# Performance work log

Hardware: AMD Instinct MI355X
Metric: run time of the kernel (lower is better)

Reference implementation:

```python
import jax, jax.numpy as jnp
import numpy as np

B, N, U = 16, 512, 128          # batch, n_node, units
E = (3 + 1) * 2                 # n_edge = (n_gaze+1)*2 with n_gaze=3
N_STEP = 3


def setup_inputs() -> dict:
    key = jax.random.key(0)
    ks = jax.random.split(key, 6)
    init_state = jax.random.normal(ks[0], (B, N, U), dtype=jnp.float32)
    adj_matrix = jax.random.uniform(ks[1], (B, E, N, N), dtype=jnp.float32)
    # learned parameters (per build()): alpha ones, w ~ N(0, 0.02), b zeros
    alpha = jnp.ones((E,), dtype=jnp.float32)
    w = jax.random.normal(ks[2], (E, U, U), dtype=jnp.float32) * 0.02
    b = jnp.zeros((E, U), dtype=jnp.float32)
    # Keras GRUCell (reset_after=False): kernel [in, 3U], recurrent [U, 3U], bias [3U]
    gru_kernel = jax.random.normal(ks[3], (E * U, 3 * U), dtype=jnp.float32) * 0.02
    gru_rec_kernel = jax.random.normal(ks[4], (U, 3 * U), dtype=jnp.float32) * 0.02
    gru_bias = jnp.zeros((3 * U,), dtype=jnp.float32)
    return {"init_state": init_state, "adj_matrix": adj_matrix, "alpha": alpha,
            "w": w, "b": b, "gru_kernel": gru_kernel,
            "gru_rec_kernel": gru_rec_kernel, "gru_bias": gru_bias}


def _gru_cell(x, h, kernel, rec, bias):
    # Keras GRUCell, reset_after=False:
    # z = sigmoid(x Wz + h Uz); r = sigmoid(x Wr + h Ur)
    # hh = tanh(x Wh + (r*h) Uh); h' = z*h + (1-z)*hh
    m = x @ kernel + bias                      # [BN, 3U]
    xz, xr, xh = jnp.split(m, 3, axis=-1)
    z = jax.nn.sigmoid(xz + h @ rec[:, :U])
    r = jax.nn.sigmoid(xr + h @ rec[:, U:2 * U])
    hh = jnp.tanh(xh + (r * h) @ rec[:, 2 * U:])
    return z * h + (1.0 - z) * hh


def reference(init_state, adj_matrix, alpha, w, b, gru_kernel, gru_rec_kernel, gru_bias):
    # contribution-coefficient weighted adjacency: [B, E, N, N]
    wadj = adj_matrix * jax.nn.sigmoid(alpha)[None, :, None, None]
    state = init_state                         # [B, N, U]
    for _ in range(N_STEP):
        # per-edge transform: h[b,n,e,u] = state[b,n,:] @ w[e] + b[e]
        h = jnp.einsum('bnd,edu->bneu', state, w) + b          # [B, N, E, U]
        # adjacency aggregation for all edges at once (fused batched GEMM)
        neigh = jnp.einsum('benm,bmeu->bneu', wadj, h)         # [B, N, E, U]
        gru_in = neigh.reshape(B * N, E * U)
        gru_h = state.reshape(B * N, U)
        state = _gru_cell(gru_in, gru_h, gru_kernel, gru_rec_kernel, gru_bias).reshape(B, N, U)
    return state
```

## Files before the change

kernel.cpp:

```cpp
#include <hip/hip_runtime.h>


typedef __attribute__((ext_vector_type(8))) short short8;
typedef __attribute__((ext_vector_type(4))) short short4v;
typedef __attribute__((ext_vector_type(4))) float f32x4;

__device__ __forceinline__ short bfs(float f) {
    __bf16 h = (__bf16)f;
    return __builtin_bit_cast(short, h);
}
__device__ __forceinline__ void split2(float x, short& hi, short& lo) {
    __bf16 h = (__bf16)x;
    hi = __builtin_bit_cast(short, h);
    __bf16 l = (__bf16)(x - (float)h);
    lo = __builtin_bit_cast(short, l);
}
__device__ __forceinline__ float sigm(float x) { return 1.0f / (1.0f + __expf(-x)); }

#define LDP 40

#define MFMA3(acc, ah, al, bh, bl)                                             \
    acc = __builtin_amdgcn_mfma_f32_16x16x32_bf16(ah, bh, acc, 0, 0, 0);       \
    acc = __builtin_amdgcn_mfma_f32_16x16x32_bf16(al, bh, acc, 0, 0, 0);       \
    acc = __builtin_amdgcn_mfma_f32_16x16x32_bf16(ah, bl, acc, 0, 0, 0);

__global__ __launch_bounds__(256) void k_prep(const float* __restrict__ w,
                                              const float* __restrict__ gk,
                                              const float* __restrict__ grk,
                                              const float* __restrict__ alpha,
                                              const float* __restrict__ init_state,
                                              short* __restrict__ Wt_hi, short* __restrict__ Wt_lo,
                                              short* __restrict__ GKt_hi, short* __restrict__ GKt_lo,
                                              short* __restrict__ REC_hi, short* __restrict__ REC_lo,
                                              short* __restrict__ NG2_hi, short* __restrict__ NG2_lo,
                                              float* __restrict__ siga) {
    int idx = blockIdx.x * 256 + threadIdx.x;
    if (idx < 131072) {
        int e = idx >> 14, rem = idx & 16383, u = rem >> 7, d = rem & 127;
        split2(w[e * 16384 + d * 128 + u], Wt_hi[idx], Wt_lo[idx]);
    } else if (idx < 573440) {
        int i2 = idx - 131072;
        int c = i2 / 1152, k = i2 - c * 1152;
        float v = (k < 1024) ? gk[k * 384 + c]
                             : ((c < 256) ? grk[(k - 1024) * 384 + c] : 0.0f);
        split2(v, GKt_hi[i2], GKt_lo[i2]);
    } else if (idx < 589824) {
        int i2 = idx - 573440;
        int u = i2 >> 7, d = i2 & 127;
        split2(grk[d * 384 + 256 + u], REC_hi[i2], REC_lo[i2]);
    } else if (idx < 1638400) {
        int i2 = idx - 589824;
        int r = i2 >> 7, d = i2 & 127;
        split2(init_state[i2], NG2_hi[(size_t)r * 1152 + 1024 + d],
                              NG2_lo[(size_t)r * 1152 + 1024 + d]);
    } else if (idx < 1638408) {
        int e = idx - 1638400;
        siga[e] = sigm(alpha[e]);
    }
}

__global__ __launch_bounds__(256) void k_edge(const short* __restrict__ Wt_hi,
                                              const short* __restrict__ Wt_lo,
                                              const short* __restrict__ NG2_hi,
                                              const short* __restrict__ NG2_lo,
                                              const float* __restrict__ bias,
                                              const float* __restrict__ siga,
                                              short* __restrict__ Ht_hi,
                                              short* __restrict__ Ht_lo) {
    const int e = blockIdx.y;
    const int col0 = blockIdx.x * 128;
    __shared__ short Ash[128 * LDP], Asl[128 * LDP];
    __shared__ short Bsh[128 * LDP], Bsl[128 * LDP];
    const int tid = threadIdx.x;
    const int lane = tid & 63, wave = tid >> 6;
    const int wr = wave >> 1, wc = wave & 1;
    const int l15 = lane & 15, g8 = (lane >> 4) * 8;
    const short* wh = Wt_hi + e * 16384;
    const short* wl = Wt_lo + e * 16384;
    f32x4 acc[4][4] = {};
    for (int k0 = 0; k0 < 128; k0 += 32) {
        __syncthreads();
#pragma unroll
        for (int it = 0; it < 2; ++it) {
            int idx = tid + it * 256;
            int r = idx >> 2, gg = idx & 3;
            *(short8*)&Ash[r * LDP + gg * 8] = *(const short8*)&wh[r * 128 + k0 + gg * 8];
            *(short8*)&Asl[r * LDP + gg * 8] = *(const short8*)&wl[r * 128 + k0 + gg * 8];
        }
#pragma unroll
        for (int it = 0; it < 2; ++it) {
            int idx = tid + it * 256;
            int r = idx >> 2, gg = idx & 3;
            size_t src = (size_t)(col0 + r) * 1152 + 1024 + k0 + gg * 8;
            *(short8*)&Bsh[r * LDP + gg * 8] = *(const short8*)&NG2_hi[src];
            *(short8*)&Bsl[r * LDP + gg * 8] = *(const short8*)&NG2_lo[src];
        }
        __syncthreads();
        short8 ah[4], al[4], bh[4], bl[4];
#pragma unroll
        for (int f = 0; f < 4; ++f) {
            int ra = (wr * 64 + f * 16 + l15) * LDP + g8;
            int rb = (wc * 64 + f * 16 + l15) * LDP + g8;
            ah[f] = *(const short8*)&Ash[ra]; al[f] = *(const short8*)&Asl[ra];
            bh[f] = *(const short8*)&Bsh[rb]; bl[f] = *(const short8*)&Bsl[rb];
        }
#pragma unroll
        for (int i = 0; i < 4; ++i)
#pragma unroll
            for (int j = 0; j < 4; ++j) { MFMA3(acc[i][j], ah[i], al[i], bh[j], bl[j]); }
    }
    const float sa = siga[e];
#pragma unroll
    for (int i = 0; i < 4; ++i) {
#pragma unroll
        for (int j = 0; j < 4; ++j) {
#pragma unroll
            for (int rg = 0; rg < 4; ++rg) {
                int u = wr * 64 + i * 16 + (lane >> 4) * 4 + rg;
                int bn = col0 + wc * 64 + j * 16 + l15;
                int b_ = bn >> 9, n = bn & 511;
                float v = sa * (acc[i][j][rg] + bias[e * 128 + u]);
                size_t o = ((size_t)(b_ * 8 + e) * 128 + u) * 512 + n;
                split2(v, Ht_hi[o], Ht_lo[o]);
            }
        }
    }
}

__global__ __launch_bounds__(256) void k_neigh(const float* __restrict__ adj,
                                               const short* __restrict__ Ht_hi,
                                               const short* __restrict__ Ht_lo,
                                               short* __restrict__ NG2_hi,
                                               short* __restrict__ NG2_lo) {
    const int be = blockIdx.y;
    const int b = be >> 3, e = be & 7;
    const int row0 = blockIdx.x * 128;
    __shared__ short Ash[128 * LDP], Asl[128 * LDP];
    __shared__ short Bsh[128 * LDP], Bsl[128 * LDP];
    const int tid = threadIdx.x;
    const int lane = tid & 63, wave = tid >> 6;
    const int wr = wave >> 1, wc = wave & 1;
    const int l15 = lane & 15, g8 = (lane >> 4) * 8;
    const float* A = adj + (size_t)be * 262144;
    const short* Bh = Ht_hi + (size_t)be * 65536;
    const short* Bl = Ht_lo + (size_t)be * 65536;
    f32x4 acc[4][4] = {};
    for (int k0 = 0; k0 < 512; k0 += 32) {
        __syncthreads();
#pragma unroll
        for (int it = 0; it < 4; ++it) {
            int idx = tid + it * 256;
            int r = idx >> 3, c4 = idx & 7;
            float4 v = *(const float4*)&A[(size_t)(row0 + r) * 512 + k0 + c4 * 4];
            short4v sh, sl;
            short h0, l0;
            split2(v.x, h0, l0); sh.x = h0; sl.x = l0;
            split2(v.y, h0, l0); sh.y = h0; sl.y = l0;
            split2(v.z, h0, l0); sh.z = h0; sl.z = l0;
            split2(v.w, h0, l0); sh.w = h0; sl.w = l0;
            *(short4v*)&Ash[r * LDP + c4 * 4] = sh;
            *(short4v*)&Asl[r * LDP + c4 * 4] = sl;
        }
#pragma unroll
        for (int it = 0; it < 2; ++it) {
            int idx = tid + it * 256;
            int r = idx >> 2, gg = idx & 3;
            *(short8*)&Bsh[r * LDP + gg * 8] = *(const short8*)&Bh[r * 512 + k0 + gg * 8];
            *(short8*)&Bsl[r * LDP + gg * 8] = *(const short8*)&Bl[r * 512 + k0 + gg * 8];
        }
        __syncthreads();
        short8 ah[4], al[4], bh[4], bl[4];
#pragma unroll
        for (int f = 0; f < 4; ++f) {
            int ra = (wr * 64 + f * 16 + l15) * LDP + g8;
            int rb = (wc * 64 + f * 16 + l15) * LDP + g8;
            ah[f] = *(const short8*)&Ash[ra]; al[f] = *(const short8*)&Asl[ra];
            bh[f] = *(const short8*)&Bsh[rb]; bl[f] = *(const short8*)&Bsl[rb];
        }
#pragma unroll
        for (int i = 0; i < 4; ++i)
#pragma unroll
            for (int j = 0; j < 4; ++j) { MFMA3(acc[i][j], ah[i], al[i], bh[j], bl[j]); }
    }
#pragma unroll
    for (int i = 0; i < 4; ++i) {
#pragma unroll
        for (int j = 0; j < 4; ++j) {
#pragma unroll
            for (int rg = 0; rg < 4; ++rg) {
                int n = row0 + wr * 64 + i * 16 + (lane >> 4) * 4 + rg;
                int u = wc * 64 + j * 16 + l15;
                size_t o = (size_t)(b * 512 + n) * 1152 + e * 128 + u;
                split2(acc[i][j][rg], NG2_hi[o], NG2_lo[o]);
            }
        }
    }
}

__global__ __launch_bounds__(256) void k_gruin(const short* __restrict__ NG2_hi,
                                               const short* __restrict__ NG2_lo,
                                               const short* __restrict__ GKt_hi,
                                               const short* __restrict__ GKt_lo,
                                               const float* __restrict__ gbias,
                                               float* __restrict__ M) {
    const int col0 = blockIdx.x * 128;
    const int row0 = blockIdx.y * 128;
    __shared__ short Ash[128 * LDP], Asl[128 * LDP];
    __shared__ short Bsh[128 * LDP], Bsl[128 * LDP];
    const int tid = threadIdx.x;
    const int lane = tid & 63, wave = tid >> 6;
    const int wr = wave >> 1, wc = wave & 1;
    const int l15 = lane & 15, g8 = (lane >> 4) * 8;
    f32x4 acc[4][4] = {};
    for (int k0 = 0; k0 < 1152; k0 += 32) {
        __syncthreads();
#pragma unroll
        for (int it = 0; it < 2; ++it) {
            int idx = tid + it * 256;
            int r = idx >> 2, gg = idx & 3;
            size_t src = (size_t)(row0 + r) * 1152 + k0 + gg * 8;
            *(short8*)&Ash[r * LDP + gg * 8] = *(const short8*)&NG2_hi[src];
            *(short8*)&Asl[r * LDP + gg * 8] = *(const short8*)&NG2_lo[src];
        }
#pragma unroll
        for (int it = 0; it < 2; ++it) {
            int idx = tid + it * 256;
            int r = idx >> 2, gg = idx & 3;
            size_t src = (size_t)(col0 + r) * 1152 + k0 + gg * 8;
            *(short8*)&Bsh[r * LDP + gg * 8] = *(const short8*)&GKt_hi[src];
            *(short8*)&Bsl[r * LDP + gg * 8] = *(const short8*)&GKt_lo[src];
        }
        __syncthreads();
        short8 ah[4], al[4], bh[4], bl[4];
#pragma unroll
        for (int f = 0; f < 4; ++f) {
            int ra = (wr * 64 + f * 16 + l15) * LDP + g8;
            int rb = (wc * 64 + f * 16 + l15) * LDP + g8;
            ah[f] = *(const short8*)&Ash[ra]; al[f] = *(const short8*)&Asl[ra];
            bh[f] = *(const short8*)&Bsh[rb]; bl[f] = *(const short8*)&Bsl[rb];
        }
#pragma unroll
        for (int i = 0; i < 4; ++i)
#pragma unroll
            for (int j = 0; j < 4; ++j) { MFMA3(acc[i][j], ah[i], al[i], bh[j], bl[j]); }
    }
#pragma unroll
    for (int i = 0; i < 4; ++i) {
#pragma unroll
        for (int j = 0; j < 4; ++j) {
#pragma unroll
            for (int rg = 0; rg < 4; ++rg) {
                int R = row0 + wr * 64 + i * 16 + (lane >> 4) * 4 + rg;
                int c = col0 + wc * 64 + j * 16 + l15;
                M[(size_t)R * 384 + c] = acc[i][j][rg] + gbias[c];
            }
        }
    }
}

__global__ __launch_bounds__(256) void k_hh(const float* __restrict__ M,
                                            const short* __restrict__ REC_hi,
                                            const short* __restrict__ REC_lo,
                                            float* __restrict__ S,
                                            short* __restrict__ NG2_hi,
                                            short* __restrict__ NG2_lo) {
    const int row0 = blockIdx.x * 128;
    __shared__ short Ash[128 * LDP], Asl[128 * LDP];
    __shared__ short Bsh[128 * LDP], Bsl[128 * LDP];
    const int tid = threadIdx.x;
    const int lane = tid & 63, wave = tid >> 6;
    const int wr = wave >> 1, wc = wave & 1;
    const int l15 = lane & 15, g8 = (lane >> 4) * 8;
    f32x4 acc[4][4] = {};
    for (int k0 = 0; k0 < 128; k0 += 32) {
        __syncthreads();
#pragma unroll
        for (int it = 0; it < 4; ++it) {
            int idx = tid + it * 256;
            int r = idx >> 3, c4 = idx & 7;
            float4 m4 = *(const float4*)&M[(size_t)(row0 + r) * 384 + 128 + k0 + c4 * 4];
            float4 h4 = *(const float4*)&S[(size_t)(row0 + r) * 128 + k0 + c4 * 4];
            short4v sh, sl;
            short h0, l0;
            split2(sigm(m4.x) * h4.x, h0, l0); sh.x = h0; sl.x = l0;
            split2(sigm(m4.y) * h4.y, h0, l0); sh.y = h0; sl.y = l0;
            split2(sigm(m4.z) * h4.z, h0, l0); sh.z = h0; sl.z = l0;
            split2(sigm(m4.w) * h4.w, h0, l0); sh.w = h0; sl.w = l0;
            *(short4v*)&Ash[r * LDP + c4 * 4] = sh;
            *(short4v*)&Asl[r * LDP + c4 * 4] = sl;
        }
#pragma unroll
        for (int it = 0; it < 2; ++it) {
            int idx = tid + it * 256;
            int r = idx >> 2, gg = idx & 3;
            *(short8*)&Bsh[r * LDP + gg * 8] = *(const short8*)&REC_hi[r * 128 + k0 + gg * 8];
            *(short8*)&Bsl[r * LDP + gg * 8] = *(const short8*)&REC_lo[r * 128 + k0 + gg * 8];
        }
        __syncthreads();
        short8 ah[4], al[4], bh[4], bl[4];
#pragma unroll
        for (int f = 0; f < 4; ++f) {
            int ra = (wr * 64 + f * 16 + l15) * LDP + g8;
            int rb = (wc * 64 + f * 16 + l15) * LDP + g8;
            ah[f] = *(const short8*)&Ash[ra]; al[f] = *(const short8*)&Asl[ra];
            bh[f] = *(const short8*)&Bsh[rb]; bl[f] = *(const short8*)&Bsl[rb];
        }
#pragma unroll
        for (int i = 0; i < 4; ++i)
#pragma unroll
            for (int j = 0; j < 4; ++j) { MFMA3(acc[i][j], ah[i], al[i], bh[j], bl[j]); }
    }
#pragma unroll
    for (int i = 0; i < 4; ++i) {
#pragma unroll
        for (int j = 0; j < 4; ++j) {
#pragma unroll
            for (int rg = 0; rg < 4; ++rg) {
                int R = row0 + wr * 64 + i * 16 + (lane >> 4) * 4 + rg;
                int u = wc * 64 + j * 16 + l15;
                float z = sigm(M[(size_t)R * 384 + u]);
                float xh = M[(size_t)R * 384 + 256 + u];
                float h = S[(size_t)R * 128 + u];
                float hh = tanhf(xh + acc[i][j][rg]);
                float sn = z * h + (1.0f - z) * hh;
                S[(size_t)R * 128 + u] = sn;
                split2(sn, NG2_hi[(size_t)R * 1152 + 1024 + u],
                           NG2_lo[(size_t)R * 1152 + 1024 + u]);
            }
        }
    }
}

extern "C" void kernel_launch(void* const* d_in, const int* in_sizes, int n_in,
                              void* d_out, int out_size, void* d_ws, size_t ws_size,
                              hipStream_t stream) {
    const float* init_state = (const float*)d_in[0];
    const float* adj        = (const float*)d_in[1];
    const float* alpha      = (const float*)d_in[2];
    const float* w          = (const float*)d_in[3];
    const float* bias       = (const float*)d_in[4];
    const float* gk         = (const float*)d_in[5];
    const float* grk        = (const float*)d_in[6];
    const float* gbias      = (const float*)d_in[7];
    float* state = (float*)d_out;

    char* ws = (char*)d_ws;
    short* NG2_hi = (short*)(ws);
    short* NG2_lo = (short*)(ws + 18874368);
    short* Ht_hi  = (short*)(ws + 37748736);
    float* M      = (float*)(ws + 37748736);
    short* Ht_lo  = (short*)(ws + 54525952);
    short* Wt_hi  = (short*)(ws + 71303168);
    short* Wt_lo  = (short*)(ws + 71565312);
    short* GKt_hi = (short*)(ws + 71827456);
    short* GKt_lo = (short*)(ws + 72712192);
    short* REC_hi = (short*)(ws + 73596928);
    short* REC_lo = (short*)(ws + 73629696);
    float* siga   = (float*)(ws + 73662464);

    k_prep<<<dim3(6401), 256, 0, stream>>>(w, gk, grk, alpha, init_state,
                                           Wt_hi, Wt_lo, GKt_hi, GKt_lo,
                                           REC_hi, REC_lo, NG2_hi, NG2_lo, siga);
    (void)hipMemcpyAsync(state, init_state, (size_t)8192 * 128 * sizeof(float),
                         hipMemcpyDeviceToDevice, stream);

    for (int step = 0; step < 3; ++step) {
        k_edge <<<dim3(64, 8),  256, 0, stream>>>(Wt_hi, Wt_lo, NG2_hi, NG2_lo,
                                                  bias, siga, Ht_hi, Ht_lo);
        k_neigh<<<dim3(4, 128), 256, 0, stream>>>(adj, Ht_hi, Ht_lo, NG2_hi, NG2_lo);
        k_gruin<<<dim3(3, 64),  256, 0, stream>>>(NG2_hi, NG2_lo, GKt_hi, GKt_lo,
                                                  gbias, M);
        k_hh   <<<dim3(64),     256, 0, stream>>>(M, REC_hi, REC_lo, state,
                                                  NG2_hi, NG2_lo);
    }
}
```

Measured before the change: 654.0 us.

## Retile k_hh into 32-row blocks with full-K LDS staging and vectorized epilogue

The k_hh kernel now handles 32 rows per block instead of 128 and launches 256 blocks instead of 64, so more of the GPU's compute units get work. Each block loads the whole 128-wide K dimension of the r*h operand and the recurrent weights into LDS once, replacing the per-32 K-loop and its repeated syncs. The GEMM result is staged through shared memory, so the GRU epilogue can use coalesced float4 loads and stores for M, S and NG2. In exchange, each block reloads the full 128x128 REC_hi/REC_lo weights and uses much more LDS per block, which may limit how many blocks fit on a compute unit at once.

```diff
diff --git a/kernel.cpp b/kernel.cpp
--- a/kernel.cpp
+++ b/kernel.cpp
@@ -18,6 +18,7 @@
 __device__ __forceinline__ float sigm(float x) { return 1.0f / (1.0f + __expf(-x)); }
 
 #define LDP 40
+#define LDH 136
 
 #define MFMA3(acc, ah, al, bh, bl)                                             \
     acc = __builtin_amdgcn_mfma_f32_16x16x32_bf16(ah, bh, acc, 0, 0, 0);       \
@@ -264,70 +265,97 @@
                                             float* __restrict__ S,
                                             short* __restrict__ NG2_hi,
                                             short* __restrict__ NG2_lo) {
-    const int row0 = blockIdx.x * 128;
-    __shared__ short Ash[128 * LDP], Asl[128 * LDP];
-    __shared__ short Bsh[128 * LDP], Bsl[128 * LDP];
+    const int row0 = blockIdx.x * 32;
+    __shared__ short Ash[32 * LDH], Asl[32 * LDH];
+    __shared__ short Bsh[128 * LDH], Bsl[128 * LDH];
+    __shared__ float hh[32][132];
     const int tid = threadIdx.x;
     const int lane = tid & 63, wave = tid >> 6;
-    const int wr = wave >> 1, wc = wave & 1;
     const int l15 = lane & 15, g8 = (lane >> 4) * 8;
-    f32x4 acc[4][4] = {};
-    for (int k0 = 0; k0 < 128; k0 += 32) {
-        __syncthreads();
-#pragma unroll
-        for (int it = 0; it < 4; ++it) {
-            int idx = tid + it * 256;
-            int r = idx >> 3, c4 = idx & 7;
-            float4 m4 = *(const float4*)&M[(size_t)(row0 + r) * 384 + 128 + k0 + c4 * 4];
-            float4 h4 = *(const float4*)&S[(size_t)(row0 + r) * 128 + k0 + c4 * 4];
-            short4v sh, sl;
-            short h0, l0;
-            split2(sigm(m4.x) * h4.x, h0, l0); sh.x = h0; sl.x = l0;
-            split2(sigm(m4.y) * h4.y, h0, l0); sh.y = h0; sl.y = l0;
-            split2(sigm(m4.z) * h4.z, h0, l0); sh.z = h0; sl.z = l0;
-            split2(sigm(m4.w) * h4.w, h0, l0); sh.w = h0; sl.w = l0;
-            *(short4v*)&Ash[r * LDP + c4 * 4] = sh;
-            *(short4v*)&Asl[r * LDP + c4 * 4] = sl;
-        }
-#pragma unroll
-        for (int it = 0; it < 2; ++it) {
-            int idx = tid + it * 256;
-            int r = idx >> 2, gg = idx & 3;
-            *(short8*)&Bsh[r * LDP + gg * 8] = *(const short8*)&REC_hi[r * 128 + k0 + gg * 8];
-            *(short8*)&Bsl[r * LDP + gg * 8] = *(const short8*)&REC_lo[r * 128 + k0 + gg * 8];
-        }
-        __syncthreads();
-        short8 ah[4], al[4], bh[4], bl[4];
-#pragma unroll
-        for (int f = 0; f < 4; ++f) {
-            int ra = (wr * 64 + f * 16 + l15) * LDP + g8;
-            int rb = (wc * 64 + f * 16 + l15) * LDP + g8;
-            ah[f] = *(const short8*)&Ash[ra]; al[f] = *(const short8*)&Asl[ra];
-            bh[f] = *(const short8*)&Bsh[rb]; bl[f] = *(const short8*)&Bsl[rb];
-        }
-#pragma unroll
-        for (int i = 0; i < 4; ++i)
-#pragma unroll
-            for (int j = 0; j < 4; ++j) { MFMA3(acc[i][j], ah[i], al[i], bh[j], bl[j]); }
-    }
-#pragma unroll
-    for (int i = 0; i < 4; ++i) {
-#pragma unroll
-        for (int j = 0; j < 4; ++j) {
+
+#pragma unroll
+    for (int g = 0; g < 4; ++g) {
+        int i2 = g * 1024 + tid * 4;
+        int r = i2 >> 7, c = i2 & 127;
+        float4 m4 = *(const float4*)&M[(size_t)(row0 + r) * 384 + 128 + c];
+        float4 h4 = *(const float4*)&S[(size_t)(row0 + r) * 128 + c];
+        short4v sh, sl;
+        short h0, l0;
+        split2(sigm(m4.x) * h4.x, h0, l0); sh.x = h0; sl.x = l0;
+        split2(sigm(m4.y) * h4.y, h0, l0); sh.y = h0; sl.y = l0;
+        split2(sigm(m4.z) * h4.z, h0, l0); sh.z = h0; sl.z = l0;
+        split2(sigm(m4.w) * h4.w, h0, l0); sh.w = h0; sl.w = l0;
+        *(short4v*)&Ash[r * LDH + c] = sh;
+        *(short4v*)&Asl[r * LDH + c] = sl;
+    }
+#pragma unroll
+    for (int it = 0; it < 8; ++it) {
+        int idx = tid + it * 256;
+        int r = idx >> 4, gg = idx & 15;
+        *(short8*)&Bsh[r * LDH + gg * 8] = *(const short8*)&REC_hi[r * 128 + gg * 8];
+        *(short8*)&Bsl[r * LDH + gg * 8] = *(const short8*)&REC_lo[r * 128 + gg * 8];
+    }
+    __syncthreads();
+
+    f32x4 acc[2][2] = {};
+#pragma unroll
+    for (int ks = 0; ks < 4; ++ks) {
+        short8 ah[2], al_[2], bh[2], bl_[2];
+#pragma unroll
+        for (int f = 0; f < 2; ++f) {
+            int ra = (f * 16 + l15) * LDH + ks * 32 + g8;
+            int rb = (wave * 32 + f * 16 + l15) * LDH + ks * 32 + g8;
+            ah[f] = *(const short8*)&Ash[ra]; al_[f] = *(const short8*)&Asl[ra];
+            bh[f] = *(const short8*)&Bsh[rb]; bl_[f] = *(const short8*)&Bsl[rb];
+        }
+#pragma unroll
+        for (int i = 0; i < 2; ++i)
+#pragma unroll
+            for (int j = 0; j < 2; ++j) { MFMA3(acc[i][j], ah[i], al_[i], bh[j], bl_[j]); }
+    }
+#pragma unroll
+    for (int i = 0; i < 2; ++i)
+#pragma unroll
+        for (int j = 0; j < 2; ++j)
 #pragma unroll
             for (int rg = 0; rg < 4; ++rg) {
-                int R = row0 + wr * 64 + i * 16 + (lane >> 4) * 4 + rg;
-                int u = wc * 64 + j * 16 + l15;
-                float z = sigm(M[(size_t)R * 384 + u]);
-                float xh = M[(size_t)R * 384 + 256 + u];
-                float h = S[(size_t)R * 128 + u];
-                float hh = tanhf(xh + acc[i][j][rg]);
-                float sn = z * h + (1.0f - z) * hh;
-                S[(size_t)R * 128 + u] = sn;
-                split2(sn, NG2_hi[(size_t)R * 1152 + 1024 + u],
-                           NG2_lo[(size_t)R * 1152 + 1024 + u]);
+                int r = i * 16 + (lane >> 4) * 4 + rg;
+                int c = wave * 32 + j * 16 + l15;
+                hh[r][c] = acc[i][j][rg];
             }
-        }
+    __syncthreads();
+
+#pragma unroll
+    for (int g = 0; g < 4; ++g) {
+        int i2 = g * 1024 + tid * 4;
+        int r = i2 >> 7, c = i2 & 127;
+        int R = row0 + r;
+        float4 z4 = *(const float4*)&M[(size_t)R * 384 + c];
+        float4 x4 = *(const float4*)&M[(size_t)R * 384 + 256 + c];
+        float4 h4 = *(const float4*)&S[(size_t)R * 128 + c];
+        float4 l4 = *(const float4*)&hh[r][c];
+        float4 sn;
+        {
+            float z = sigm(z4.x); sn.x = z * h4.x + (1.0f - z) * tanhf(x4.x + l4.x);
+        }
+        {
+            float z = sigm(z4.y); sn.y = z * h4.y + (1.0f - z) * tanhf(x4.y + l4.y);
+        }
+        {
+            float z = sigm(z4.z); sn.z = z * h4.z + (1.0f - z) * tanhf(x4.z + l4.z);
+        }
+        {
+            float z = sigm(z4.w); sn.w = z * h4.w + (1.0f - z) * tanhf(x4.w + l4.w);
+        }
+        *(float4*)&S[(size_t)R * 128 + c] = sn;
+        short4v sh, sl;
+        short h0, l0;
+        split2(sn.x, h0, l0); sh.x = h0; sl.x = l0;
+        split2(sn.y, h0, l0); sh.y = h0; sl.y = l0;
+        split2(sn.z, h0, l0); sh.z = h0; sl.z = l0;
+        split2(sn.w, h0, l0); sh.w = h0; sl.w = l0;
+        *(short4v*)&NG2_hi[(size_t)R * 1152 + 1024 + c] = sh;
+        *(short4v*)&NG2_lo[(size_t)R * 1152 + 1024 + c] = sl;
     }
 }
 
@@ -370,7 +398,7 @@
         k_neigh<<<dim3(4, 128), 256, 0, stream>>>(adj, Ht_hi, Ht_lo, NG2_hi, NG2_lo);
         k_gruin<<<dim3(3, 64),  256, 0, stream>>>(NG2_hi, NG2_lo, GKt_hi, GKt_lo,
                                                   gbias, M);
-        k_hh   <<<dim3(64),     256, 0, stream>>>(M, REC_hi, REC_lo, state,
+        k_hh   <<<dim3(256),    256, 0, stream>>>(M, REC_hi, REC_lo, state,
                                                   NG2_hi, NG2_lo);
     }
 }
```

Result: faster. 587.3 us (-10.2%).

## Retile k_hh to 16-row blocks for more parallelism across CUs

Applied to the files above, without the earlier changes.

The recurrent-hidden GEMM kernel k_hh is retiled from 128x128 output tiles on 64 blocks to 16-row tiles on 512 blocks. Each wave now computes a 16x32 slice over the full K=128 in one pass, and the B operand (REC) is read directly from global/L2 instead of being staged in shared memory. The goal is to fill far more of the GPU's CUs, since 64 blocks leave most of them idle. In exchange, REC is reloaded by every block and per-block data reuse is lower.

```diff
diff --git a/kernel.cpp b/kernel.cpp
--- a/kernel.cpp
+++ b/kernel.cpp
@@ -18,6 +18,7 @@
 __device__ __forceinline__ float sigm(float x) { return 1.0f / (1.0f + __expf(-x)); }
 
 #define LDP 40
+#define LDH 136
 
 #define MFMA3(acc, ah, al, bh, bl)                                             \
     acc = __builtin_amdgcn_mfma_f32_16x16x32_bf16(ah, bh, acc, 0, 0, 0);       \
@@ -264,69 +265,57 @@
                                             float* __restrict__ S,
                                             short* __restrict__ NG2_hi,
                                             short* __restrict__ NG2_lo) {
-    const int row0 = blockIdx.x * 128;
-    __shared__ short Ash[128 * LDP], Asl[128 * LDP];
-    __shared__ short Bsh[128 * LDP], Bsl[128 * LDP];
+    const int row0 = blockIdx.x * 16;
+    __shared__ short Ash[16 * LDH], Asl[16 * LDH];
     const int tid = threadIdx.x;
     const int lane = tid & 63, wave = tid >> 6;
-    const int wr = wave >> 1, wc = wave & 1;
     const int l15 = lane & 15, g8 = (lane >> 4) * 8;
-    f32x4 acc[4][4] = {};
-    for (int k0 = 0; k0 < 128; k0 += 32) {
-        __syncthreads();
-#pragma unroll
-        for (int it = 0; it < 4; ++it) {
-            int idx = tid + it * 256;
-            int r = idx >> 3, c4 = idx & 7;
-            float4 m4 = *(const float4*)&M[(size_t)(row0 + r) * 384 + 128 + k0 + c4 * 4];
-            float4 h4 = *(const float4*)&S[(size_t)(row0 + r) * 128 + k0 + c4 * 4];
-            short4v sh, sl;
-            short h0, l0;
-            split2(sigm(m4.x) * h4.x, h0, l0); sh.x = h0; sl.x = l0;
-            split2(sigm(m4.y) * h4.y, h0, l0); sh.y = h0; sl.y = l0;
-            split2(sigm(m4.z) * h4.z, h0, l0); sh.z = h0; sl.z = l0;
-            split2(sigm(m4.w) * h4.w, h0, l0); sh.w = h0; sl.w = l0;
-            *(short4v*)&Ash[r * LDP + c4 * 4] = sh;
-            *(short4v*)&Asl[r * LDP + c4 * 4] = sl;
-        }
-#pragma unroll
-        for (int it = 0; it < 2; ++it) {
-            int idx = tid + it * 256;
-            int r = idx >> 2, gg = idx & 3;
-            *(short8*)&Bsh[r * LDP + gg * 8] = *(const short8*)&REC_hi[r * 128 + k0 + gg * 8];
-            *(short8*)&Bsl[r * LDP + gg * 8] = *(const short8*)&REC_lo[r * 128 + k0 + gg * 8];
-        }
-        __syncthreads();
-        short8 ah[4], al[4], bh[4], bl[4];
-#pragma unroll
-        for (int f = 0; f < 4; ++f) {
-            int ra = (wr * 64 + f * 16 + l15) * LDP + g8;
-            int rb = (wc * 64 + f * 16 + l15) * LDP + g8;
-            ah[f] = *(const short8*)&Ash[ra]; al[f] = *(const short8*)&Asl[ra];
-            bh[f] = *(const short8*)&Bsh[rb]; bl[f] = *(const short8*)&Bsl[rb];
-        }
-#pragma unroll
-        for (int i = 0; i < 4; ++i)
-#pragma unroll
-            for (int j = 0; j < 4; ++j) { MFMA3(acc[i][j], ah[i], al[i], bh[j], bl[j]); }
-    }
-#pragma unroll
-    for (int i = 0; i < 4; ++i) {
-#pragma unroll
-        for (int j = 0; j < 4; ++j) {
-#pragma unroll
-            for (int rg = 0; rg < 4; ++rg) {
-                int R = row0 + wr * 64 + i * 16 + (lane >> 4) * 4 + rg;
-                int u = wc * 64 + j * 16 + l15;
-                float z = sigm(M[(size_t)R * 384 + u]);
-                float xh = M[(size_t)R * 384 + 256 + u];
-                float h = S[(size_t)R * 128 + u];
-                float hh = tanhf(xh + acc[i][j][rg]);
-                float sn = z * h + (1.0f - z) * hh;
-                S[(size_t)R * 128 + u] = sn;
-                split2(sn, NG2_hi[(size_t)R * 1152 + 1024 + u],
-                           NG2_lo[(size_t)R * 1152 + 1024 + u]);
-            }
+    const int u0 = wave * 32;
+
+#pragma unroll
+    for (int g = 0; g < 2; ++g) {
+        int i2 = g * 1024 + tid * 4;
+        int r = i2 >> 7, c = i2 & 127;
+        float4 m4 = *(const float4*)&M[(size_t)(row0 + r) * 384 + 128 + c];
+        float4 h4 = *(const float4*)&S[(size_t)(row0 + r) * 128 + c];
+        short4v sh, sl;
+        short h0, l0;
+        split2(sigm(m4.x) * h4.x, h0, l0); sh.x = h0; sl.x = l0;
+        split2(sigm(m4.y) * h4.y, h0, l0); sh.y = h0; sl.y = l0;
+        split2(sigm(m4.z) * h4.z, h0, l0); sh.z = h0; sl.z = l0;
+        split2(sigm(m4.w) * h4.w, h0, l0); sh.w = h0; sl.w = l0;
+        *(short4v*)&Ash[r * LDH + c] = sh;
+        *(short4v*)&Asl[r * LDH + c] = sl;
+    }
+    __syncthreads();
+
+    f32x4 acc[2] = {};
+#pragma unroll
+    for (int ks = 0; ks < 4; ++ks) {
+        short8 ah = *(const short8*)&Ash[l15 * LDH + ks * 32 + g8];
+        short8 al = *(const short8*)&Asl[l15 * LDH + ks * 32 + g8];
+#pragma unroll
+        for (int j = 0; j < 2; ++j) {
+            int urow = u0 + j * 16 + l15;
+            short8 bh = *(const short8*)&REC_hi[urow * 128 + ks * 32 + g8];
+            short8 bl = *(const short8*)&REC_lo[urow * 128 + ks * 32 + g8];
+            MFMA3(acc[j], ah, al, bh, bl);
+        }
+    }
+
+#pragma unroll
+    for (int j = 0; j < 2; ++j) {
+#pragma unroll
+        for (int rg = 0; rg < 4; ++rg) {
+            int R = row0 + (lane >> 4) * 4 + rg;
+            int u = u0 + j * 16 + l15;
+            float z = sigm(M[(size_t)R * 384 + u]);
+            float xh = M[(size_t)R * 384 + 256 + u];
+            float h = S[(size_t)R * 128 + u];
+            float sn = z * h + (1.0f - z) * tanhf(xh + acc[j][rg]);
+            S[(size_t)R * 128 + u] = sn;
+            split2(sn, NG2_hi[(size_t)R * 1152 + 1024 + u],
+                       NG2_lo[(size_t)R * 1152 + 1024 + u]);
         }
     }
 }
@@ -370,7 +359,7 @@
         k_neigh<<<dim3(4, 128), 256, 0, stream>>>(adj, Ht_hi, Ht_lo, NG2_hi, NG2_lo);
         k_gruin<<<dim3(3, 64),  256, 0, stream>>>(NG2_hi, NG2_lo, GKt_hi, GKt_lo,
                                                   gbias, M);
-        k_hh   <<<dim3(64),     256, 0, stream>>>(M, REC_hi, REC_lo, state,
+        k_hh   <<<dim3(512),    256, 0, stream>>>(M, REC_hi, REC_lo, state,
                                                   NG2_hi, NG2_lo);
     }
 }
```

After: 589.3 us. 9.9% less time.
